# Performance work log

Measured on AMD Instinct MI355X. Metric: run time of the kernel, lower is better.

## Reference

```python
import jax, jax.numpy as jnp
import numpy as np

CAP = 512  # per-expert capacity; mean tokens/expert = 4096*4/64 = 256, CAP = mean + ~16 sigma (no drops for seed 0)


def _moe_forward(hidden_states, gate_w, w13, w2, top_k):
    T, H = hidden_states.shape
    E = gate_w.shape[0]
    # --- gating: softmax over expert logits, then top-k (npu_moe_gating_top_k_softmax) ---
    logits = hidden_states @ gate_w.T                      # [T, E]
    probs = jax.nn.softmax(logits, axis=-1)
    topk_w, topk_idx = jax.lax.top_k(probs, top_k)         # [T, K]
    # norm_topk_prob=True and top_k > 1
    topk_w = topk_w / (topk_w.sum(axis=-1, keepdims=True) + 1e-20)
    # --- init_routing: compute each (token, slot)'s rank within its expert ---
    N = T * top_k
    flat_e = topk_idx.reshape(N)                           # [N] expert id per expanded row
    order = jnp.argsort(flat_e)                            # stable sort by expert
    sorted_e = flat_e[order]
    counts = jax.ops.segment_sum(jnp.ones((N,), jnp.int32), flat_e, num_segments=E)
    starts = jnp.cumsum(counts) - counts                   # [E] start offset of each expert group
    rank_sorted = jnp.arange(N, dtype=jnp.int32) - starts[sorted_e].astype(jnp.int32)
    rank = jnp.zeros((N,), jnp.int32).at[order].set(rank_sorted)  # within-expert position
    # --- dispatch into [E, CAP, H] buffers (token gather/scatter) ---
    x_rep = jnp.repeat(hidden_states, top_k, axis=0)       # [N, H]
    disp = jnp.zeros((E, CAP, H), hidden_states.dtype).at[flat_e, rank].set(x_rep)
    # --- grouped GEMM: SwiGLU expert FFN as batched matmuls ---
    h = jnp.einsum('ech,ehf->ecf', disp, w13)              # [E, CAP, 2I]
    g, u = jnp.split(h, 2, axis=-1)
    a = jax.nn.silu(g) * u                                 # [E, CAP, I]
    y = jnp.einsum('eci,eih->ech', a, w2)                  # [E, CAP, H]
    # --- finalize_routing: gather back and weighted combine ---
    out_rows = y[flat_e, rank]                             # [N, H]
    out = (out_rows.reshape(T, top_k, H) * topk_w[..., None]).sum(axis=1)
    return out


def setup_inputs() -> dict:
    key = jax.random.key(0)
    k1, k2, k3, k4 = jax.random.split(key, 4)
    T, H, E, I = 4096, 2048, 64, 768
    hidden_states = jax.random.normal(k1, (T, H), dtype=jnp.float32)
    gate_w = jax.random.normal(k2, (E, H), dtype=jnp.float32) * 0.02
    w13 = jax.random.normal(k3, (E, H, 2 * I), dtype=jnp.float32) * 0.02
    w2 = jax.random.normal(k4, (E, I, H), dtype=jnp.float32) * 0.02
    return {"hidden_states": hidden_states, "gate_w": gate_w, "w13": w13, "w2": w2, "top_k": 4}


def reference(hidden_states, gate_w, w13, w2, top_k):
    return _moe_forward(hidden_states, gate_w, w13, w2, top_k)
```

## Files before the change

### kernel.cpp

```cpp
#include <hip/hip_runtime.h>
#include <hip/hip_bf16.h>

#define T_TOK 4096
#define HDIM  2048
#define NEXP  64
#define IDIM  768
#define TOPK  4
#define CAPE  512
#define NFLAT (T_TOK*TOPK)

typedef __bf16        bf16x8 __attribute__((ext_vector_type(8)));
typedef float         f32x4  __attribute__((ext_vector_type(4)));
typedef unsigned int  u32x4  __attribute__((ext_vector_type(4)));

__device__ __forceinline__ unsigned short f2bf(float f) {
  __bf16 b = (__bf16)f;
  return __builtin_bit_cast(unsigned short, b);
}
__device__ __forceinline__ unsigned pack2(float lo, float hi) {
  return (unsigned)f2bf(lo) | ((unsigned)f2bf(hi) << 16);
}
__device__ __forceinline__ int swz(int row, int chunk) {
  return row*128 + (((chunk ^ (row & 7) ^ ((row >> 3) & 7)) & 7) << 4);
}

__global__ __launch_bounds__(256) void k_gating(
    const float* __restrict__ hs, const float* __restrict__ gw,
    unsigned short* __restrict__ hs_bf, int* __restrict__ tidx, float* __restrict__ tw)
{
  __shared__ float lg[16][64];
  const int tid = threadIdx.x;
  const int t0  = blockIdx.x * 16;

  {
    const f32x4* src = (const f32x4*)(hs + (size_t)t0 * HDIM);
    for (int i = tid; i < 16 * HDIM / 4; i += 256) {
      f32x4 v = src[i];
      ushort4 o;
      o.x = f2bf(v[0]); o.y = f2bf(v[1]); o.z = f2bf(v[2]); o.w = f2bf(v[3]);
      *(ushort4*)(hs_bf + (size_t)t0 * HDIM + (size_t)i * 4) = o;
    }
  }

  const int lane = tid & 63, wv = tid >> 6;
  {
    const f32x4* gr = (const f32x4*)(gw + (size_t)lane * HDIM);
    const f32x4* x0 = (const f32x4*)(hs + (size_t)(t0 + wv*4 + 0) * HDIM);
    const f32x4* x1 = (const f32x4*)(hs + (size_t)(t0 + wv*4 + 1) * HDIM);
    const f32x4* x2 = (const f32x4*)(hs + (size_t)(t0 + wv*4 + 2) * HDIM);
    const f32x4* x3 = (const f32x4*)(hs + (size_t)(t0 + wv*4 + 3) * HDIM);
    float a0=0.f, a1=0.f, a2=0.f, a3=0.f;
    for (int h = 0; h < HDIM/4; ++h) {
      f32x4 g = gr[h];
      f32x4 v0 = x0[h], v1 = x1[h], v2 = x2[h], v3 = x3[h];
      a0 += g[0]*v0[0] + g[1]*v0[1] + g[2]*v0[2] + g[3]*v0[3];
      a1 += g[0]*v1[0] + g[1]*v1[1] + g[2]*v1[2] + g[3]*v1[3];
      a2 += g[0]*v2[0] + g[1]*v2[1] + g[2]*v2[2] + g[3]*v2[3];
      a3 += g[0]*v3[0] + g[1]*v3[1] + g[2]*v3[2] + g[3]*v3[3];
    }
    lg[wv*4+0][lane] = a0;
    lg[wv*4+1][lane] = a1;
    lg[wv*4+2][lane] = a2;
    lg[wv*4+3][lane] = a3;
  }
  __syncthreads();

  if (tid < 16) {
    const int t = t0 + tid;
    unsigned long long chosen = 0ull;
    float bv[4]; int bi[4];
#pragma unroll
    for (int k = 0; k < 4; ++k) {
      float best = -1e30f; int b = 0;
      for (int e = 0; e < 64; ++e) {
        float v = lg[tid][e];
        if (!((chosen >> e) & 1ull) && v > best) { best = v; b = e; }
      }
      chosen |= 1ull << b; bv[k] = best; bi[k] = b;
    }
    float s = 0.f, w[4];
#pragma unroll
    for (int k = 0; k < 4; ++k) { w[k] = __expf(bv[k] - bv[0]); s += w[k]; }
    float inv = 1.f / s;
#pragma unroll
    for (int k = 0; k < 4; ++k) { tidx[t*4+k] = bi[k]; tw[t*4+k] = w[k] * inv; }
  }
}

__global__ __launch_bounds__(64) void k_count_rank(
    const int* __restrict__ tidx, int* __restrict__ rankb, int* __restrict__ counts)
{
  const int e = blockIdx.x;
  const int lane = threadIdx.x;
  int base = 0;
  for (int c = 0; c < NFLAT/64; ++c) {
    int n = c*64 + lane;
    bool m = (tidx[n] == e);
    unsigned long long mask = __ballot(m);
    if (m) rankb[n] = base + __popcll(mask & ((1ull << lane) - 1ull));
    base += __popcll(mask);
  }
  if (lane == 0) counts[e] = base;
}

__global__ __launch_bounds__(256) void k_build(
    const int* __restrict__ tidx, const int* __restrict__ rankb,
    const int* __restrict__ counts,
    int* __restrict__ starts, int* __restrict__ row_info, int* __restrict__ sortpos)
{
  __shared__ int s_starts[NEXP];
  if (threadIdx.x == 0) {
    int s = 0;
    for (int e = 0; e < NEXP; ++e) { s_starts[e] = s; starts[e] = s; s += counts[e]; }
  }
  __syncthreads();
  for (int n = threadIdx.x; n < NFLAT; n += 256) {
    int e = tidx[n], r = rankb[n];
    int sr = s_starts[e] + r;
    row_info[sr] = n;
    sortpos[n] = (r < CAPE) ? sr : -1;
  }
}

__global__ __launch_bounds__(512, 2) void k_gemm1(
    const unsigned short* __restrict__ hs_bf, const float* __restrict__ w13,
    const int* __restrict__ counts, const int* __restrict__ starts,
    const int* __restrict__ row_info, unsigned short* __restrict__ a_buf)
{
  const int nt = blockIdx.x;
  const int e  = blockIdx.y;
  const int count = min(counts[e], CAPE);
  if (count <= 0) return;
  const int nmt = (count + 255) >> 8;
  const int tid = threadIdx.x;
  const int estart = starts[e];

  __shared__ __align__(16) char lds[2*65536];

  const int mrow = tid >> 3, cchunk = tid & 7;
  const float* w13e = w13 + (size_t)e * HDIM * (2*IDIM);
  const int half = tid >> 8;
  const int t8   = tid & 255;
  const int kg   = t8 >> 5;
  const int n4   = (t8 & 31) * 4;
  const int lane = tid & 63, wv = tid >> 6;
  const int wr = wv >> 1, wc = wv & 1;

  int cur = 0;
  for (int mi = 0; mi < nmt; ++mi) {
    const int R0 = mi << 8;
    const int base_sorted = estart + R0;
    int tokp[4];
#pragma unroll
    for (int p = 0; p < 4; ++p) {
      int sr = base_sorted + mrow + p*64;
      if (sr > NFLAT-1) sr = NFLAT-1;
      tokp[p] = row_info[sr] >> 2;
    }
    f32x4 accg[4][4], accu[4][4];
#pragma unroll
    for (int i = 0; i < 4; ++i)
#pragma unroll
      for (int j = 0; j < 4; ++j) { accg[i][j] = f32x4{0.f,0.f,0.f,0.f}; accu[i][j] = f32x4{0.f,0.f,0.f,0.f}; }

    u32x4 rA[4]; f32x4 rB[8];
#pragma unroll
    for (int p = 0; p < 4; ++p)
      rA[p] = *(const u32x4*)(hs_bf + (size_t)tokp[p]*HDIM + cchunk*8);
    {
      const float* bp = w13e + (size_t)(kg*8) * (2*IDIM) + half*IDIM + nt*128 + n4;
#pragma unroll
      for (int j = 0; j < 8; ++j) rB[j] = *(const f32x4*)(bp + (size_t)j * (2*IDIM));
    }
    __syncthreads();
    {
      char* A0 = lds + cur*65536;
      char* B0 = lds + cur*65536 + 32768 + half*16384;
#pragma unroll
      for (int p = 0; p < 4; ++p)
        *(u32x4*)(A0 + swz(mrow + p*64, cchunk)) = rA[p];
#pragma unroll
      for (int i = 0; i < 4; ++i) {
        u32x4 q;
        q[0] = pack2(rB[0][i], rB[1][i]);
        q[1] = pack2(rB[2][i], rB[3][i]);
        q[2] = pack2(rB[4][i], rB[5][i]);
        q[3] = pack2(rB[6][i], rB[7][i]);
        *(u32x4*)(B0 + swz(n4 + i, kg)) = q;
      }
    }

    for (int kt = 0; kt < HDIM/64; ++kt) {
      __syncthreads();
      const bool pf = (kt+1 < HDIM/64);
      if (pf) {
#pragma unroll
        for (int p = 0; p < 4; ++p)
          rA[p] = *(const u32x4*)(hs_bf + (size_t)tokp[p]*HDIM + (kt+1)*64 + cchunk*8);
        const float* bp = w13e + (size_t)((kt+1)*64 + kg*8) * (2*IDIM) + half*IDIM + nt*128 + n4;
#pragma unroll
        for (int j = 0; j < 8; ++j) rB[j] = *(const f32x4*)(bp + (size_t)j * (2*IDIM));
      }
      char* Ac  = lds + cur*65536;
      char* Bgc = lds + cur*65536 + 32768;
      char* Buc = Bgc + 16384;
#pragma unroll
      for (int kfi = 0; kfi < 2; ++kfi) {
        const int ch = (kfi<<2) | (lane>>4);
        bf16x8 af[4], bg[4], bu[4];
#pragma unroll
        for (int mi2 = 0; mi2 < 4; ++mi2) {
          int row = wr*64 + mi2*16 + (lane & 15);
          af[mi2] = *(const bf16x8*)(Ac + swz(row, ch));
        }
#pragma unroll
        for (int ni = 0; ni < 4; ++ni) {
          int n = wc*64 + ni*16 + (lane & 15);
          bg[ni] = *(const bf16x8*)(Bgc + swz(n, ch));
          bu[ni] = *(const bf16x8*)(Buc + swz(n, ch));
        }
#pragma unroll
        for (int mi2 = 0; mi2 < 4; ++mi2)
#pragma unroll
          for (int ni = 0; ni < 4; ++ni) {
            accg[mi2][ni] = __builtin_amdgcn_mfma_f32_16x16x32_bf16(af[mi2], bg[ni], accg[mi2][ni], 0, 0, 0);
            accu[mi2][ni] = __builtin_amdgcn_mfma_f32_16x16x32_bf16(af[mi2], bu[ni], accu[mi2][ni], 0, 0, 0);
          }
      }
      if (pf) {
        char* An = lds + (cur^1)*65536;
        char* Bn = lds + (cur^1)*65536 + 32768 + half*16384;
#pragma unroll
        for (int p = 0; p < 4; ++p)
          *(u32x4*)(An + swz(mrow + p*64, cchunk)) = rA[p];
#pragma unroll
        for (int i = 0; i < 4; ++i) {
          u32x4 q;
          q[0] = pack2(rB[0][i], rB[1][i]);
          q[1] = pack2(rB[2][i], rB[3][i]);
          q[2] = pack2(rB[4][i], rB[5][i]);
          q[3] = pack2(rB[6][i], rB[7][i]);
          *(u32x4*)(Bn + swz(n4 + i, kg)) = q;
        }
      }
      cur ^= 1;
    }

#pragma unroll
    for (int mi2 = 0; mi2 < 4; ++mi2) {
#pragma unroll
      for (int j = 0; j < 4; ++j) {
        int rl = wr*64 + mi2*16 + (lane >> 4)*4 + j;
        if (R0 + rl < count) {
          size_t rowoff = (size_t)(base_sorted + rl) * IDIM;
#pragma unroll
          for (int ni = 0; ni < 4; ++ni) {
            int col = nt*128 + wc*64 + ni*16 + (lane & 15);
            float g = accg[mi2][ni][j], u = accu[mi2][ni][j];
            float a = (g / (1.f + __expf(-g))) * u;
            a_buf[rowoff + col] = f2bf(a);
          }
        }
      }
    }
  }
}

__global__ __launch_bounds__(512, 2) void k_gemm2(
    const unsigned short* __restrict__ a_buf, const float* __restrict__ w2,
    const int* __restrict__ counts, const int* __restrict__ starts,
    unsigned short* __restrict__ y_buf)
{
  const int nt = blockIdx.x;
  const int e  = blockIdx.y;
  const int count = min(counts[e], CAPE);
  if (count <= 0) return;
  const int nmt = (count + 255) >> 8;
  const int tid = threadIdx.x;
  const int estart = starts[e];

  __shared__ __align__(16) char lds[2*65536];

  const int mrow = tid >> 3, cchunk = tid & 7;
  const float* w2e = w2 + (size_t)e * IDIM * HDIM;
  const int pass = tid >> 8;
  const int t8   = tid & 255;
  const int kg   = t8 >> 5, n4 = (t8 & 31) * 4;
  const int lane = tid & 63, wv = tid >> 6, wr = wv >> 1, wc = wv & 1;

  int cur = 0;
  for (int mi = 0; mi < nmt; ++mi) {
    const int R0 = mi << 8;
    const int base_sorted = estart + R0;
    int srp[4];
#pragma unroll
    for (int p = 0; p < 4; ++p) {
      int sr = base_sorted + mrow + p*64;
      srp[p] = (sr > NFLAT-1) ? (NFLAT-1) : sr;
    }
    f32x4 acc[4][8];
#pragma unroll
    for (int i = 0; i < 4; ++i)
#pragma unroll
      for (int j = 0; j < 8; ++j) acc[i][j] = f32x4{0.f,0.f,0.f,0.f};

    u32x4 rA[4]; f32x4 rB[8];
#pragma unroll
    for (int p = 0; p < 4; ++p)
      rA[p] = *(const u32x4*)(a_buf + (size_t)srp[p]*IDIM + cchunk*8);
    {
      const float* bp = w2e + (size_t)(kg*8) * HDIM + nt*256 + pass*128 + n4;
#pragma unroll
      for (int j = 0; j < 8; ++j) rB[j] = *(const f32x4*)(bp + (size_t)j * HDIM);
    }
    __syncthreads();
    {
      char* A0 = lds + cur*65536;
      char* B0 = lds + cur*65536 + 32768;
#pragma unroll
      for (int p = 0; p < 4; ++p)
        *(u32x4*)(A0 + swz(mrow + p*64, cchunk)) = rA[p];
#pragma unroll
      for (int i = 0; i < 4; ++i) {
        int n = pass*128 + n4 + i;
        u32x4 q;
        q[0] = pack2(rB[0][i], rB[1][i]);
        q[1] = pack2(rB[2][i], rB[3][i]);
        q[2] = pack2(rB[4][i], rB[5][i]);
        q[3] = pack2(rB[6][i], rB[7][i]);
        *(u32x4*)(B0 + swz(n, kg)) = q;
      }
    }

    for (int kt = 0; kt < IDIM/64; ++kt) {
      __syncthreads();
      const bool pf = (kt+1 < IDIM/64);
      if (pf) {
#pragma unroll
        for (int p = 0; p < 4; ++p)
          rA[p] = *(const u32x4*)(a_buf + (size_t)srp[p]*IDIM + (kt+1)*64 + cchunk*8);
        const float* bp = w2e + (size_t)((kt+1)*64 + kg*8) * HDIM + nt*256 + pass*128 + n4;
#pragma unroll
        for (int j = 0; j < 8; ++j) rB[j] = *(const f32x4*)(bp + (size_t)j * HDIM);
      }
      char* Ac = lds + cur*65536;
      char* Bc = lds + cur*65536 + 32768;
#pragma unroll
      for (int kfi = 0; kfi < 2; ++kfi) {
        const int ch = (kfi<<2) | (lane>>4);
        bf16x8 af[4], bb[8];
#pragma unroll
        for (int mi2 = 0; mi2 < 4; ++mi2) {
          int row = wr*64 + mi2*16 + (lane & 15);
          af[mi2] = *(const bf16x8*)(Ac + swz(row, ch));
        }
#pragma unroll
        for (int ni = 0; ni < 8; ++ni) {
          int n = wc*128 + ni*16 + (lane & 15);
          bb[ni] = *(const bf16x8*)(Bc + swz(n, ch));
        }
#pragma unroll
        for (int mi2 = 0; mi2 < 4; ++mi2)
#pragma unroll
          for (int ni = 0; ni < 8; ++ni)
            acc[mi2][ni] = __builtin_amdgcn_mfma_f32_16x16x32_bf16(af[mi2], bb[ni], acc[mi2][ni], 0, 0, 0);
      }
      if (pf) {
        char* An = lds + (cur^1)*65536;
        char* Bn = lds + (cur^1)*65536 + 32768;
#pragma unroll
        for (int p = 0; p < 4; ++p)
          *(u32x4*)(An + swz(mrow + p*64, cchunk)) = rA[p];
#pragma unroll
        for (int i = 0; i < 4; ++i) {
          int n = pass*128 + n4 + i;
          u32x4 q;
          q[0] = pack2(rB[0][i], rB[1][i]);
          q[1] = pack2(rB[2][i], rB[3][i]);
          q[2] = pack2(rB[4][i], rB[5][i]);
          q[3] = pack2(rB[6][i], rB[7][i]);
          *(u32x4*)(Bn + swz(n, kg)) = q;
        }
      }
      cur ^= 1;
    }

#pragma unroll
    for (int mi2 = 0; mi2 < 4; ++mi2) {
#pragma unroll
      for (int j = 0; j < 4; ++j) {
        int rl = wr*64 + mi2*16 + (lane >> 4)*4 + j;
        if (R0 + rl < count) {
          int sr = base_sorted + rl;
          unsigned short* yrow = y_buf + (size_t)sr * HDIM;
#pragma unroll
          for (int ni = 0; ni < 8; ++ni) {
            int col = nt*256 + wc*128 + ni*16 + (lane & 15);
            yrow[col] = f2bf(acc[mi2][ni][j]);
          }
        }
      }
    }
  }
}

__global__ __launch_bounds__(256) void k_finalize(
    const unsigned short* __restrict__ y_buf, const int* __restrict__ sortpos,
    const float* __restrict__ tw, float* __restrict__ out)
{
  const int t = blockIdx.x;
  const int tid = threadIdx.x;
  float acc[8];
#pragma unroll
  for (int i = 0; i < 8; ++i) acc[i] = 0.f;
#pragma unroll
  for (int k = 0; k < 4; ++k) {
    int sp = sortpos[t*4+k];
    float w = tw[t*4+k];
    if (sp >= 0) {
      u32x4 v = *(const u32x4*)(y_buf + (size_t)sp * HDIM + tid*8);
#pragma unroll
      for (int q = 0; q < 4; ++q) {
        float lo = __builtin_bit_cast(float, v[q] << 16);
        float hi = __builtin_bit_cast(float, v[q] & 0xffff0000u);
        acc[2*q]   += w * lo;
        acc[2*q+1] += w * hi;
      }
    }
  }
  f32x4 o0 = {acc[0], acc[1], acc[2], acc[3]};
  f32x4 o1 = {acc[4], acc[5], acc[6], acc[7]};
  f32x4* o = (f32x4*)(out + (size_t)t * HDIM + tid*8);
  o[0] = o0;
  o[1] = o1;
}

extern "C" void kernel_launch(void* const* d_in, const int* in_sizes, int n_in,
                              void* d_out, int out_size, void* d_ws, size_t ws_size,
                              hipStream_t stream) {
  const float* hs  = (const float*)d_in[0];
  const float* gw  = (const float*)d_in[1];
  const float* w13 = (const float*)d_in[2];
  const float* w2  = (const float*)d_in[3];
  float* out = (float*)d_out;

  char* ws = (char*)d_ws;
  size_t off = 0;
  auto alloc = [&](size_t bytes) {
    off = (off + 255) & ~(size_t)255;
    char* p = ws + off;
    off += bytes;
    return p;
  };
  unsigned short* hs_bf = (unsigned short*)alloc((size_t)T_TOK * HDIM * 2);
  int*   tidx   = (int*)  alloc((size_t)NFLAT * 4);
  float* tw     = (float*)alloc((size_t)NFLAT * 4);
  int*   rankb  = (int*)  alloc((size_t)NFLAT * 4);
  int*   counts = (int*)  alloc((size_t)NEXP * 4);
  int*   starts = (int*)  alloc((size_t)NEXP * 4);
  int*   rinfo  = (int*)  alloc((size_t)NFLAT * 4);
  int*   sortp  = (int*)  alloc((size_t)NFLAT * 4);
  unsigned short* a_buf = (unsigned short*)alloc((size_t)NFLAT * IDIM * 2);
  unsigned short* y_buf = (unsigned short*)alloc((size_t)NFLAT * HDIM * 2);
  (void)ws_size; (void)in_sizes; (void)n_in; (void)out_size;

  k_gating<<<T_TOK/16, 256, 0, stream>>>(hs, gw, hs_bf, tidx, tw);
  k_count_rank<<<NEXP, 64, 0, stream>>>(tidx, rankb, counts);
  k_build<<<1, 256, 0, stream>>>(tidx, rankb, counts, starts, rinfo, sortp);
  k_gemm1<<<dim3(6, NEXP), 512, 0, stream>>>(hs_bf, w13, counts, starts, rinfo, a_buf);
  k_gemm2<<<dim3(8, NEXP), 512, 0, stream>>>(a_buf, w2, counts, starts, y_buf);
  k_finalize<<<T_TOK, 256, 0, stream>>>(y_buf, sortp, tw, out);
}
```

Baseline: 886.4 us.

## Restructure GEMM k-loop pipeline with single lightweight barrier and MFMA priority

Both expert GEMM kernels now issue global loads for tile k+2 right after the barrier that follows the LDS stores for tile k+1. The global-memory prefetch therefore stays in flight across the next MFMA phase. The __syncthreads calls are replaced by a custom barrier that waits only on LDS counters, not outstanding vector-memory loads, and there is one barrier per iteration. s_setprio raises wave priority around the MFMA block so math issues ahead of memory work from other waves. The intent is to hide global-load latency and cut barrier stalls, at the cost of more delicate ordering that relies on the compiler inserting vmcnt waits before the register data is stored.

```diff
diff --git a/kernel.cpp b/kernel.cpp
--- a/kernel.cpp
+++ b/kernel.cpp
@@ -22,6 +22,10 @@
 }
 __device__ __forceinline__ int swz(int row, int chunk) {
   return row*128 + (((chunk ^ (row & 7) ^ ((row >> 3) & 7)) & 7) << 4);
+}
+__device__ __forceinline__ void wg_barrier() {
+  asm volatile("s_waitcnt lgkmcnt(0)" ::: "memory");
+  __builtin_amdgcn_s_barrier();
 }
 
 __global__ __launch_bounds__(256) void k_gating(
@@ -134,6 +138,7 @@
   const int nmt = (count + 255) >> 8;
   const int tid = threadIdx.x;
   const int estart = starts[e];
+  const int NK = HDIM/64;
 
   __shared__ __align__(16) char lds[2*65536];
 
@@ -145,8 +150,8 @@
   const int n4   = (t8 & 31) * 4;
   const int lane = tid & 63, wv = tid >> 6;
   const int wr = wv >> 1, wc = wv & 1;
-
-  int cur = 0;
+  const float* bbase = w13e + (size_t)(kg*8) * (2*IDIM) + half*IDIM + nt*128 + n4;
+
   for (int mi = 0; mi < nmt; ++mi) {
     const int R0 = mi << 8;
     const int base_sorted = estart + R0;
@@ -167,15 +172,11 @@
 #pragma unroll
     for (int p = 0; p < 4; ++p)
       rA[p] = *(const u32x4*)(hs_bf + (size_t)tokp[p]*HDIM + cchunk*8);
+#pragma unroll
+    for (int j = 0; j < 8; ++j) rB[j] = *(const f32x4*)(bbase + (size_t)j * (2*IDIM));
     {
-      const float* bp = w13e + (size_t)(kg*8) * (2*IDIM) + half*IDIM + nt*128 + n4;
-#pragma unroll
-      for (int j = 0; j < 8; ++j) rB[j] = *(const f32x4*)(bp + (size_t)j * (2*IDIM));
-    }
-    __syncthreads();
-    {
-      char* A0 = lds + cur*65536;
-      char* B0 = lds + cur*65536 + 32768 + half*16384;
+      char* A0 = lds;
+      char* B0 = lds + 32768 + half*16384;
 #pragma unroll
       for (int p = 0; p < 4; ++p)
         *(u32x4*)(A0 + swz(mrow + p*64, cchunk)) = rA[p];
@@ -189,30 +190,26 @@
         *(u32x4*)(B0 + swz(n4 + i, kg)) = q;
       }
     }
-
-    for (int kt = 0; kt < HDIM/64; ++kt) {
-      __syncthreads();
-      const bool pf = (kt+1 < HDIM/64);
-      if (pf) {
-#pragma unroll
-        for (int p = 0; p < 4; ++p)
-          rA[p] = *(const u32x4*)(hs_bf + (size_t)tokp[p]*HDIM + (kt+1)*64 + cchunk*8);
-        const float* bp = w13e + (size_t)((kt+1)*64 + kg*8) * (2*IDIM) + half*IDIM + nt*128 + n4;
-#pragma unroll
-        for (int j = 0; j < 8; ++j) rB[j] = *(const f32x4*)(bp + (size_t)j * (2*IDIM));
-      }
+    wg_barrier();
+#pragma unroll
+    for (int p = 0; p < 4; ++p)
+      rA[p] = *(const u32x4*)(hs_bf + (size_t)tokp[p]*HDIM + 64 + cchunk*8);
+#pragma unroll
+    for (int j = 0; j < 8; ++j) rB[j] = *(const f32x4*)(bbase + 64*(2*IDIM) + (size_t)j * (2*IDIM));
+
+    int cur = 0;
+    for (int kt = 0; kt < NK; ++kt) {
       char* Ac  = lds + cur*65536;
-      char* Bgc = lds + cur*65536 + 32768;
+      char* Bgc = Ac + 32768;
       char* Buc = Bgc + 16384;
+      __builtin_amdgcn_s_setprio(1);
 #pragma unroll
       for (int kfi = 0; kfi < 2; ++kfi) {
         const int ch = (kfi<<2) | (lane>>4);
         bf16x8 af[4], bg[4], bu[4];
 #pragma unroll
-        for (int mi2 = 0; mi2 < 4; ++mi2) {
-          int row = wr*64 + mi2*16 + (lane & 15);
-          af[mi2] = *(const bf16x8*)(Ac + swz(row, ch));
-        }
+        for (int m2 = 0; m2 < 4; ++m2)
+          af[m2] = *(const bf16x8*)(Ac + swz(wr*64 + m2*16 + (lane & 15), ch));
 #pragma unroll
         for (int ni = 0; ni < 4; ++ni) {
           int n = wc*64 + ni*16 + (lane & 15);
@@ -220,16 +217,17 @@
           bu[ni] = *(const bf16x8*)(Buc + swz(n, ch));
         }
 #pragma unroll
-        for (int mi2 = 0; mi2 < 4; ++mi2)
+        for (int m2 = 0; m2 < 4; ++m2)
 #pragma unroll
           for (int ni = 0; ni < 4; ++ni) {
-            accg[mi2][ni] = __builtin_amdgcn_mfma_f32_16x16x32_bf16(af[mi2], bg[ni], accg[mi2][ni], 0, 0, 0);
-            accu[mi2][ni] = __builtin_amdgcn_mfma_f32_16x16x32_bf16(af[mi2], bu[ni], accu[mi2][ni], 0, 0, 0);
+            accg[m2][ni] = __builtin_amdgcn_mfma_f32_16x16x32_bf16(af[m2], bg[ni], accg[m2][ni], 0, 0, 0);
+            accu[m2][ni] = __builtin_amdgcn_mfma_f32_16x16x32_bf16(af[m2], bu[ni], accu[m2][ni], 0, 0, 0);
           }
       }
-      if (pf) {
+      __builtin_amdgcn_s_setprio(0);
+      if (kt+1 < NK) {
         char* An = lds + (cur^1)*65536;
-        char* Bn = lds + (cur^1)*65536 + 32768 + half*16384;
+        char* Bn = An + 32768 + half*16384;
 #pragma unroll
         for (int p = 0; p < 4; ++p)
           *(u32x4*)(An + swz(mrow + p*64, cchunk)) = rA[p];
@@ -243,20 +241,29 @@
           *(u32x4*)(Bn + swz(n4 + i, kg)) = q;
         }
       }
+      wg_barrier();
+      if (kt+2 < NK) {
+#pragma unroll
+        for (int p = 0; p < 4; ++p)
+          rA[p] = *(const u32x4*)(hs_bf + (size_t)tokp[p]*HDIM + (kt+2)*64 + cchunk*8);
+        const float* bp = bbase + (size_t)(kt+2)*64 * (2*IDIM);
+#pragma unroll
+        for (int j = 0; j < 8; ++j) rB[j] = *(const f32x4*)(bp + (size_t)j * (2*IDIM));
+      }
       cur ^= 1;
     }
 
 #pragma unroll
-    for (int mi2 = 0; mi2 < 4; ++mi2) {
+    for (int m2 = 0; m2 < 4; ++m2) {
 #pragma unroll
       for (int j = 0; j < 4; ++j) {
-        int rl = wr*64 + mi2*16 + (lane >> 4)*4 + j;
+        int rl = wr*64 + m2*16 + (lane >> 4)*4 + j;
         if (R0 + rl < count) {
           size_t rowoff = (size_t)(base_sorted + rl) * IDIM;
 #pragma unroll
           for (int ni = 0; ni < 4; ++ni) {
             int col = nt*128 + wc*64 + ni*16 + (lane & 15);
-            float g = accg[mi2][ni][j], u = accu[mi2][ni][j];
+            float g = accg[m2][ni][j], u = accu[m2][ni][j];
             float a = (g / (1.f + __expf(-g))) * u;
             a_buf[rowoff + col] = f2bf(a);
           }
@@ -278,6 +285,7 @@
   const int nmt = (count + 255) >> 8;
   const int tid = threadIdx.x;
   const int estart = starts[e];
+  const int NK = IDIM/64;
 
   __shared__ __align__(16) char lds[2*65536];
 
@@ -287,8 +295,8 @@
   const int t8   = tid & 255;
   const int kg   = t8 >> 5, n4 = (t8 & 31) * 4;
   const int lane = tid & 63, wv = tid >> 6, wr = wv >> 1, wc = wv & 1;
-
-  int cur = 0;
+  const float* bbase = w2e + (size_t)(kg*8) * HDIM + nt*256 + pass*128 + n4;
+
   for (int mi = 0; mi < nmt; ++mi) {
     const int R0 = mi << 8;
     const int base_sorted = estart + R0;
@@ -308,15 +316,11 @@
 #pragma unroll
     for (int p = 0; p < 4; ++p)
       rA[p] = *(const u32x4*)(a_buf + (size_t)srp[p]*IDIM + cchunk*8);
+#pragma unroll
+    for (int j = 0; j < 8; ++j) rB[j] = *(const f32x4*)(bbase + (size_t)j * HDIM);
     {
-      const float* bp = w2e + (size_t)(kg*8) * HDIM + nt*256 + pass*128 + n4;
-#pragma unroll
-      for (int j = 0; j < 8; ++j) rB[j] = *(const f32x4*)(bp + (size_t)j * HDIM);
-    }
-    __syncthreads();
-    {
-      char* A0 = lds + cur*65536;
-      char* B0 = lds + cur*65536 + 32768;
+      char* A0 = lds;
+      char* B0 = lds + 32768;
 #pragma unroll
       for (int p = 0; p < 4; ++p)
         *(u32x4*)(A0 + swz(mrow + p*64, cchunk)) = rA[p];
@@ -331,43 +335,40 @@
         *(u32x4*)(B0 + swz(n, kg)) = q;
       }
     }
-
-    for (int kt = 0; kt < IDIM/64; ++kt) {
-      __syncthreads();
-      const bool pf = (kt+1 < IDIM/64);
-      if (pf) {
-#pragma unroll
-        for (int p = 0; p < 4; ++p)
-          rA[p] = *(const u32x4*)(a_buf + (size_t)srp[p]*IDIM + (kt+1)*64 + cchunk*8);
-        const float* bp = w2e + (size_t)((kt+1)*64 + kg*8) * HDIM + nt*256 + pass*128 + n4;
-#pragma unroll
-        for (int j = 0; j < 8; ++j) rB[j] = *(const f32x4*)(bp + (size_t)j * HDIM);
-      }
+    wg_barrier();
+#pragma unroll
+    for (int p = 0; p < 4; ++p)
+      rA[p] = *(const u32x4*)(a_buf + (size_t)srp[p]*IDIM + 64 + cchunk*8);
+#pragma unroll
+    for (int j = 0; j < 8; ++j) rB[j] = *(const f32x4*)(bbase + 64*HDIM + (size_t)j * HDIM);
+
+    int cur = 0;
+    for (int kt = 0; kt < NK; ++kt) {
       char* Ac = lds + cur*65536;
-      char* Bc = lds + cur*65536 + 32768;
+      char* Bc = Ac + 32768;
+      __builtin_amdgcn_s_setprio(1);
 #pragma unroll
       for (int kfi = 0; kfi < 2; ++kfi) {
         const int ch = (kfi<<2) | (lane>>4);
         bf16x8 af[4], bb[8];
 #pragma unroll
-        for (int mi2 = 0; mi2 < 4; ++mi2) {
-          int row = wr*64 + mi2*16 + (lane & 15);
-          af[mi2] = *(const bf16x8*)(Ac + swz(row, ch));
-        }
+        for (int m2 = 0; m2 < 4; ++m2)
+          af[m2] = *(const bf16x8*)(Ac + swz(wr*64 + m2*16 + (lane & 15), ch));
 #pragma unroll
         for (int ni = 0; ni < 8; ++ni) {
           int n = wc*128 + ni*16 + (lane & 15);
           bb[ni] = *(const bf16x8*)(Bc + swz(n, ch));
         }
 #pragma unroll
-        for (int mi2 = 0; mi2 < 4; ++mi2)
+        for (int m2 = 0; m2 < 4; ++m2)
 #pragma unroll
           for (int ni = 0; ni < 8; ++ni)
-            acc[mi2][ni] = __builtin_amdgcn_mfma_f32_16x16x32_bf16(af[mi2], bb[ni], acc[mi2][ni], 0, 0, 0);
-      }
-      if (pf) {
+            acc[m2][ni] = __builtin_amdgcn_mfma_f32_16x16x32_bf16(af[m2], bb[ni], acc[m2][ni], 0, 0, 0);
+      }
+      __builtin_amdgcn_s_setprio(0);
+      if (kt+1 < NK) {
         char* An = lds + (cur^1)*65536;
-        char* Bn = lds + (cur^1)*65536 + 32768;
+        char* Bn = An + 32768;
 #pragma unroll
         for (int p = 0; p < 4; ++p)
           *(u32x4*)(An + swz(mrow + p*64, cchunk)) = rA[p];
@@ -382,21 +383,30 @@
           *(u32x4*)(Bn + swz(n, kg)) = q;
         }
       }
+      wg_barrier();
+      if (kt+2 < NK) {
+#pragma unroll
+        for (int p = 0; p < 4; ++p)
+          rA[p] = *(const u32x4*)(a_buf + (size_t)srp[p]*IDIM + (kt+2)*64 + cchunk*8);
+        const float* bp = bbase + (size_t)(kt+2)*64 * HDIM;
+#pragma unroll
+        for (int j = 0; j < 8; ++j) rB[j] = *(const f32x4*)(bp + (size_t)j * HDIM);
+      }
       cur ^= 1;
     }
 
 #pragma unroll
-    for (int mi2 = 0; mi2 < 4; ++mi2) {
+    for (int m2 = 0; m2 < 4; ++m2) {
 #pragma unroll
       for (int j = 0; j < 4; ++j) {
-        int rl = wr*64 + mi2*16 + (lane >> 4)*4 + j;
+        int rl = wr*64 + m2*16 + (lane >> 4)*4 + j;
         if (R0 + rl < count) {
           int sr = base_sorted + rl;
           unsigned short* yrow = y_buf + (size_t)sr * HDIM;
 #pragma unroll
           for (int ni = 0; ni < 8; ++ni) {
             int col = nt*256 + wc*128 + ni*16 + (lane & 15);
-            yrow[col] = f2bf(acc[mi2][ni][j]);
+            yrow[col] = f2bf(acc[m2][ni][j]);
           }
         }
       }
```

Result: slower. 1.419 ms (+60.1%).
